# Optimization experiments

Hardware: AMD Instinct MI355X
Metric: run time of the kernel (lower is better)

Reference implementation:

```python
import jax, jax.numpy as jnp
import numpy as np

B, C, N = 16, 32, 131072


def setup_inputs() -> dict:
    key = jax.random.key(0)
    k1, k2 = jax.random.split(key)
    pred = jax.random.normal(k1, (B, C, N), dtype=jnp.float32)
    true = jax.random.randint(k2, (B, N), 0, C, dtype=jnp.int32)
    return {"pred": pred, "true": true}


def reference(pred, true):
    """FPCELossV3.

    Torch loop semantics: for class i, pos_i are the point indices n (over ALL
    batch rows, with multiplicity) where true[b', n] == i; the term
    -log(p)/p at pred[b, i, n] is summed over every batch b and every such
    occurrence. Equivalent to weighting f(pred[b, i, n]) by
    count[i, n] = sum_{b'} [true[b', n] == i].
    """
    Bc, Cc, Nc = pred.shape
    logp = jax.nn.log_softmax(pred, axis=1)          # (B,C,N)
    p = jnp.exp(logp)
    f = -logp / p                                    # -log(p)/p, (B,C,N)
    # count[c, n] = number of batch rows b' with true[b', n] == c
    counts = jnp.sum(jax.nn.one_hot(true, Cc, dtype=pred.dtype), axis=0).T  # (C,N)
    loss = jnp.sum(f * counts[None, :, :]) / Nc
    return loss
```

## Files before the change

### kernel.cpp

```cpp
#include <hip/hip_runtime.h>


#define B_TOT   16
#define C_CLS   32
#define BSPLIT  8
#define VEC     2
#define TPB     256

typedef float v2f __attribute__((ext_vector_type(2)));
typedef int   v2i __attribute__((ext_vector_type(2)));

__global__ __launch_bounds__(TPB) void fpce_partial(
    const float* __restrict__ pred, const int* __restrict__ tru,
    float* __restrict__ partial, int N) {
  const int half = blockIdx.x & 1;
  const int nb   = blockIdx.x >> 1;
  const int b0   = half * BSPLIT;
  const int n0   = nb * (TPB * VEC) + threadIdx.x * VEC;

  unsigned tp[VEC][4];
#pragma unroll
  for (int w = 0; w < 4; ++w) {
    v2i r0 = *(const v2i*)(tru + (size_t)(4 * w + 0) * N + n0);
    v2i r1 = *(const v2i*)(tru + (size_t)(4 * w + 1) * N + n0);
    v2i r2 = *(const v2i*)(tru + (size_t)(4 * w + 2) * N + n0);
    v2i r3 = *(const v2i*)(tru + (size_t)(4 * w + 3) * N + n0);
#pragma unroll
    for (int k = 0; k < VEC; ++k)
      tp[k][w] =  (unsigned)r0[k]        | ((unsigned)r1[k] << 8)
               | ((unsigned)r2[k] << 16) | ((unsigned)r3[k] << 24);
  }

  float S[BSPLIT][VEC], T0[BSPLIT][VEC], T1[BSPLIT][VEC];
#pragma unroll
  for (int j = 0; j < BSPLIT; ++j)
#pragma unroll
    for (int k = 0; k < VEC; ++k) { S[j][k] = 0.f; T0[j][k] = 0.f; T1[j][k] = 0.f; }

  const float* pj[BSPLIT];
#pragma unroll
  for (int j = 0; j < BSPLIT; ++j)
    pj[j] = pred + (size_t)(b0 + j) * C_CLS * N + n0;

  for (int c = 0; c < C_CLS; ++c) {
    v2f x[BSPLIT];
#pragma unroll
    for (int j = 0; j < BSPLIT; ++j)
      x[j] = *(const v2f*)pj[j];

    const unsigned m = (unsigned)c * 0x01010101u;
    float cf[VEC];
#pragma unroll
    for (int k = 0; k < VEC; ++k) {
      unsigned n1 = 0;
#pragma unroll
      for (int w = 0; w < 4; ++w) {
        const unsigned u = (tp[k][w] ^ m) + 0x7f7f7f7fu;
        n1 += (unsigned)__popc(u & 0x80808080u);
      }
      cf[k] = (float)(B_TOT - (int)n1);
    }

#pragma unroll
    for (int j = 0; j < BSPLIT; ++j)
#pragma unroll
      for (int k = 0; k < VEC; ++k) {
        const float xe = x[j][k];
        const float e  = __expf(xe);
        S[j][k] += e;
        const float r  = __expf(-xe);
        const float u  = cf[k] * r;
        T0[j][k] += u;
        T1[j][k]  = fmaf(u, xe, T1[j][k]);
      }

#pragma unroll
    for (int j = 0; j < BSPLIT; ++j) pj[j] += N;
  }

  float W = 0.f;
#pragma unroll
  for (int j = 0; j < BSPLIT; ++j)
#pragma unroll
    for (int k = 0; k < VEC; ++k) {
      const float L = __logf(S[j][k]);
      W += S[j][k] * (L * T0[j][k] - T1[j][k]);
    }

#pragma unroll
  for (int off = 32; off > 0; off >>= 1) W += __shfl_down(W, off, 64);

  __shared__ float swave[TPB / 64];
  const int lane = threadIdx.x & 63;
  const int wid  = threadIdx.x >> 6;
  if (lane == 0) swave[wid] = W;
  __syncthreads();
  if (threadIdx.x == 0)
    partial[blockIdx.x] = swave[0] + swave[1] + swave[2] + swave[3];
}

__global__ __launch_bounds__(TPB) void fpce_final(
    const float* __restrict__ partial, float* __restrict__ out,
    int nblocks, float invN) {
  float v = 0.f;
  for (int i = threadIdx.x; i < nblocks; i += TPB) v += partial[i];
#pragma unroll
  for (int off = 32; off > 0; off >>= 1) v += __shfl_down(v, off, 64);
  __shared__ float sw[TPB / 64];
  const int lane = threadIdx.x & 63;
  const int wid  = threadIdx.x >> 6;
  if (lane == 0) sw[wid] = v;
  __syncthreads();
  if (threadIdx.x == 0)
    out[0] = (sw[0] + sw[1] + sw[2] + sw[3]) * invN;
}

extern "C" void kernel_launch(void* const* d_in, const int* in_sizes, int n_in,
                              void* d_out, int out_size, void* d_ws, size_t ws_size,
                              hipStream_t stream) {
  const float* pred = (const float*)d_in[0];
  const int*   tru  = (const int*)d_in[1];
  float*       out  = (float*)d_out;
  float*       part = (float*)d_ws;

  const int N    = in_sizes[1] / B_TOT;
  const int nblk = (N / (TPB * VEC)) * (B_TOT / BSPLIT);

  fpce_partial<<<nblk, TPB, 0, stream>>>(pred, tru, part, N);
  fpce_final<<<1, TPB, 0, stream>>>(part, out, nblk, 1.0f / (float)N);
}
```

Measured before the change: 424.2 us.

## Precompute per-class byte counts in separate kernel; one batch row per block

Splits the work into a count kernel that writes per-(class, point) counts as bytes to workspace, then a main kernel where each block handles one batch row with 4-wide vector loads. This removes the per-block recomputation of the popcount-based class counts and the label reloads. It allows higher occupancy through smaller register state per thread. In exchange it adds a kernel launch and an extra 4 MB write plus repeated byte-count reads, with 16 row blocks each rereading the counts.

```diff
diff --git a/kernel.cpp b/kernel.cpp
--- a/kernel.cpp
+++ b/kernel.cpp
@@ -3,53 +3,33 @@
 
 #define B_TOT   16
 #define C_CLS   32
-#define BSPLIT  8
-#define VEC     2
+#define VEC     4
 #define TPB     256
 
-typedef float v2f __attribute__((ext_vector_type(2)));
-typedef int   v2i __attribute__((ext_vector_type(2)));
+typedef float v4f __attribute__((ext_vector_type(4)));
+typedef int   v4i __attribute__((ext_vector_type(4)));
 
-__global__ __launch_bounds__(TPB) void fpce_partial(
-    const float* __restrict__ pred, const int* __restrict__ tru,
-    float* __restrict__ partial, int N) {
-  const int half = blockIdx.x & 1;
-  const int nb   = blockIdx.x >> 1;
-  const int b0   = half * BSPLIT;
-  const int n0   = nb * (TPB * VEC) + threadIdx.x * VEC;
+__global__ __launch_bounds__(TPB) void fpce_counts(
+    const int* __restrict__ tru, unsigned char* __restrict__ cnt8, int N) {
+  const int n0 = (blockIdx.x * TPB + threadIdx.x) * VEC;
 
   unsigned tp[VEC][4];
 #pragma unroll
   for (int w = 0; w < 4; ++w) {
-    v2i r0 = *(const v2i*)(tru + (size_t)(4 * w + 0) * N + n0);
-    v2i r1 = *(const v2i*)(tru + (size_t)(4 * w + 1) * N + n0);
-    v2i r2 = *(const v2i*)(tru + (size_t)(4 * w + 2) * N + n0);
-    v2i r3 = *(const v2i*)(tru + (size_t)(4 * w + 3) * N + n0);
+    v4i r0 = *(const v4i*)(tru + (size_t)(4 * w + 0) * N + n0);
+    v4i r1 = *(const v4i*)(tru + (size_t)(4 * w + 1) * N + n0);
+    v4i r2 = *(const v4i*)(tru + (size_t)(4 * w + 2) * N + n0);
+    v4i r3 = *(const v4i*)(tru + (size_t)(4 * w + 3) * N + n0);
 #pragma unroll
     for (int k = 0; k < VEC; ++k)
       tp[k][w] =  (unsigned)r0[k]        | ((unsigned)r1[k] << 8)
                | ((unsigned)r2[k] << 16) | ((unsigned)r3[k] << 24);
   }
 
-  float S[BSPLIT][VEC], T0[BSPLIT][VEC], T1[BSPLIT][VEC];
 #pragma unroll
-  for (int j = 0; j < BSPLIT; ++j)
-#pragma unroll
-    for (int k = 0; k < VEC; ++k) { S[j][k] = 0.f; T0[j][k] = 0.f; T1[j][k] = 0.f; }
-
-  const float* pj[BSPLIT];
-#pragma unroll
-  for (int j = 0; j < BSPLIT; ++j)
-    pj[j] = pred + (size_t)(b0 + j) * C_CLS * N + n0;
-
   for (int c = 0; c < C_CLS; ++c) {
-    v2f x[BSPLIT];
-#pragma unroll
-    for (int j = 0; j < BSPLIT; ++j)
-      x[j] = *(const v2f*)pj[j];
-
     const unsigned m = (unsigned)c * 0x01010101u;
-    float cf[VEC];
+    unsigned packed = 0;
 #pragma unroll
     for (int k = 0; k < VEC; ++k) {
       unsigned n1 = 0;
@@ -58,34 +38,55 @@
         const unsigned u = (tp[k][w] ^ m) + 0x7f7f7f7fu;
         n1 += (unsigned)__popc(u & 0x80808080u);
       }
-      cf[k] = (float)(B_TOT - (int)n1);
+      packed |= (unsigned)(B_TOT - (int)n1) << (8 * k);
     }
+    *(unsigned*)(cnt8 + (size_t)c * N + n0) = packed;
+  }
+}
 
+__global__ __launch_bounds__(TPB, 8) void fpce_partial(
+    const float* __restrict__ pred, const unsigned char* __restrict__ cnt8,
+    float* __restrict__ partial, int N) {
+  const int b  = blockIdx.x & (B_TOT - 1);
+  const int nb = blockIdx.x >> 4;
+  const int n0 = nb * (TPB * VEC) + threadIdx.x * VEC;
+
+  const float*         p  = pred + (size_t)b * C_CLS * N + n0;
+  const unsigned char* cb = cnt8 + n0;
+
+  float S[VEC], T0[VEC], T1[VEC];
 #pragma unroll
-    for (int j = 0; j < BSPLIT; ++j)
+  for (int k = 0; k < VEC; ++k) { S[k] = 0.f; T0[k] = 0.f; T1[k] = 0.f; }
+
+#pragma unroll 4
+  for (int c = 0; c < C_CLS; ++c) {
+    const v4f      x  = *(const v4f*)p;
+    const unsigned cw = *(const unsigned*)cb;
+
+    const float cf[VEC] = { (float)(cw & 0xffu),
+                            (float)((cw >> 8)  & 0xffu),
+                            (float)((cw >> 16) & 0xffu),
+                            (float)( cw >> 24        ) };
 #pragma unroll
-      for (int k = 0; k < VEC; ++k) {
-        const float xe = x[j][k];
-        const float e  = __expf(xe);
-        S[j][k] += e;
-        const float r  = __expf(-xe);
-        const float u  = cf[k] * r;
-        T0[j][k] += u;
-        T1[j][k]  = fmaf(u, xe, T1[j][k]);
-      }
-
-#pragma unroll
-    for (int j = 0; j < BSPLIT; ++j) pj[j] += N;
+    for (int k = 0; k < VEC; ++k) {
+      const float xe = x[k];
+      const float e  = __expf(xe);
+      S[k] += e;
+      const float r  = __expf(-xe);
+      const float u  = cf[k] * r;
+      T0[k] += u;
+      T1[k]  = fmaf(u, xe, T1[k]);
+    }
+    p  += N;
+    cb += N;
   }
 
   float W = 0.f;
 #pragma unroll
-  for (int j = 0; j < BSPLIT; ++j)
-#pragma unroll
-    for (int k = 0; k < VEC; ++k) {
-      const float L = __logf(S[j][k]);
-      W += S[j][k] * (L * T0[j][k] - T1[j][k]);
-    }
+  for (int k = 0; k < VEC; ++k) {
+    const float L = __logf(S[k]);
+    W += S[k] * (L * T0[k] - T1[k]);
+  }
 
 #pragma unroll
   for (int off = 32; off > 0; off >>= 1) W += __shfl_down(W, off, 64);
@@ -121,11 +122,16 @@
   const float* pred = (const float*)d_in[0];
   const int*   tru  = (const int*)d_in[1];
   float*       out  = (float*)d_out;
-  float*       part = (float*)d_ws;
 
-  const int N    = in_sizes[1] / B_TOT;
-  const int nblk = (N / (TPB * VEC)) * (B_TOT / BSPLIT);
+  const int N = in_sizes[1] / B_TOT;
 
-  fpce_partial<<<nblk, TPB, 0, stream>>>(pred, tru, part, N);
-  fpce_final<<<1, TPB, 0, stream>>>(part, out, nblk, 1.0f / (float)N);
+  unsigned char* cnt8 = (unsigned char*)d_ws;
+  float*         part = (float*)((char*)d_ws + (size_t)C_CLS * N);
+
+  const int cblk = N / (TPB * VEC);
+  const int nblk = cblk * B_TOT;
+
+  fpce_counts <<<cblk, TPB, 0, stream>>>(tru, cnt8, N);
+  fpce_partial<<<nblk, TPB, 0, stream>>>(pred, cnt8, part, N);
+  fpce_final  <<<1,    TPB, 0, stream>>>(part, out, nblk, 1.0f / (float)N);
 }
```

Result: faster. 378.5 us (-10.8%).
